# Performance work log

Measured on AMD Instinct MI355X. Metric: run time of the kernel, lower is better.

The kernel has to match this reference:

```python
import jax, jax.numpy as jnp
import numpy as np

N = 100000
E = 1600000
IN_C, HID_C, OUT_C = 128, 128, 64


def setup_inputs() -> dict:
    key = jax.random.key(0)
    k1, k2, k3, k4, k5, k6 = jax.random.split(key, 6)
    x = jax.random.normal(k1, (N, IN_C), dtype=jnp.float32)
    edge_index = jax.random.randint(k2, (2, E), 0, N, dtype=jnp.int64)
    # Glorot-style init like PyG GCNConv Linear
    W1 = jax.random.normal(k3, (IN_C, HID_C), dtype=jnp.float32) / np.sqrt(IN_C)
    b1 = jnp.zeros((HID_C,), dtype=jnp.float32)
    W2 = jax.random.normal(k4, (HID_C, OUT_C), dtype=jnp.float32) / np.sqrt(HID_C)
    b2 = jnp.zeros((OUT_C,), dtype=jnp.float32)
    return {"x": x, "edge_index": edge_index, "W1": W1, "b1": b1, "W2": W2, "b2": b2}


def gcn_conv(x, src, dst, norm, W, b, n_nodes):
    # x: [N, F_in]; src/dst/norm: [E+N] (self-loops included)
    h = x @ W                                   # [N, F_out] small GEMM
    msg = h[src] * norm[:, None]                # [E+N, F_out] gather (dominant)
    out = jax.ops.segment_sum(msg, dst, num_segments=n_nodes)  # scatter-add
    return out + b


def gcn_norm(edge_index, n_nodes):
    # add self-loops, then symmetric normalization D^-1/2 (A+I) D^-1/2
    loop = jnp.arange(n_nodes, dtype=edge_index.dtype)
    src = jnp.concatenate([edge_index[0], loop])
    dst = jnp.concatenate([edge_index[1], loop])
    deg = jax.ops.segment_sum(jnp.ones_like(dst, dtype=jnp.float32), dst,
                              num_segments=n_nodes)
    dinv = jnp.where(deg > 0, jax.lax.rsqrt(jnp.maximum(deg, 1.0)), 0.0)
    norm = dinv[src] * dinv[dst]
    return src, dst, norm


def reference(x, edge_index, W1, b1, W2, b2):
    n_nodes = x.shape[0]
    src, dst, norm = gcn_norm(edge_index, n_nodes)  # cached=True -> computed once
    h = gcn_conv(x, src, dst, norm, W1, b1, n_nodes)
    h = jax.nn.relu(h)
    # dropout in eval mode (training=False) is identity
    out = gcn_conv(h, src, dst, norm, W2, b2, n_nodes)
    return out
```

## Files before the change

### kernel.cpp

```cpp
#include <hip/hip_runtime.h>
#include <hip/hip_fp16.h>

constexpr int NN  = 100000;
constexpr int NE  = 1600000;
constexpr int TOT = NE + NN;

constexpr int NBUK    = (NN + 255) / 256;
constexpr int EBLOCKS = 512;
constexpr int EPB     = NE / EBLOCKS;

__device__ inline float2 h2f2(unsigned int u) {
  __half2 h = __builtin_bit_cast(__half2, u);
  return __half22float2(h);
}
__device__ inline unsigned int f2h2(float a, float b) {
  __half2 h = __floats2half2_rn(a, b);
  return __builtin_bit_cast(unsigned int, h);
}

__global__ __launch_bounds__(256) void k_detect(const unsigned int* __restrict__ ei, int* __restrict__ flag) {
  __shared__ int nz;
  if (threadIdx.x == 0) nz = 0;
  __syncthreads();
  if (ei[threadIdx.x * 2 + 1] != 0u) atomicAdd(&nz, 1);
  __syncthreads();
  if (threadIdx.x == 0) flag[0] = (nz == 0) ? 1 : 0;
}

__device__ inline int load_idx(const void* ei, long long i, int is64) {
  return is64 ? (int)((const long long*)ei)[i] : ((const int*)ei)[i];
}


__global__ __launch_bounds__(256) void k_hist(const void* __restrict__ ei, const int* __restrict__ flag,
                                              int* __restrict__ hist_g) {
  __shared__ int h[NBUK];
  int is64 = flag[0];
  for (int i = threadIdx.x; i < NBUK; i += 256) h[i] = 0;
  __syncthreads();
  int e0 = blockIdx.x * EPB;
  for (int e = e0 + threadIdx.x; e < e0 + EPB; e += 256) {
    int d = load_idx(ei, (long long)NE + e, is64);
    atomicAdd(&h[d >> 8], 1);
  }
  __syncthreads();
  for (int i = threadIdx.x; i < NBUK; i += 256)
    hist_g[i * EBLOCKS + blockIdx.x] = h[i];
}

__global__ __launch_bounds__(512) void k_scan_hist(int* __restrict__ hist_g, int* __restrict__ bucket_total) {
  __shared__ int s[EBLOCKS];
  int b = blockIdx.x, t = threadIdx.x;
  int v = hist_g[b * EBLOCKS + t];
  s[t] = v;
  __syncthreads();
  for (int off = 1; off < EBLOCKS; off <<= 1) {
    int u = (t >= off) ? s[t - off] : 0;
    __syncthreads();
    s[t] += u;
    __syncthreads();
  }
  hist_g[b * EBLOCKS + t] = s[t] - v;
  if (t == EBLOCKS - 1) bucket_total[b] = s[t];
}

__global__ __launch_bounds__(512) void k_scan_buckets(const int* __restrict__ bucket_total,
                                                      int* __restrict__ edge_base, int* __restrict__ row_start) {
  __shared__ int s[512];
  int t = threadIdx.x;
  int v = (t < NBUK) ? bucket_total[t] : 0;
  s[t] = v;
  __syncthreads();
  for (int off = 1; off < 512; off <<= 1) {
    int u = (t >= off) ? s[t - off] : 0;
    __syncthreads();
    s[t] += u;
    __syncthreads();
  }
  if (t <= NBUK) edge_base[t] = s[t] - v;
  if (t == 0) row_start[NN] = TOT;
}

__global__ __launch_bounds__(256) void k_scatter(const void* __restrict__ ei, const int* __restrict__ flag,
                                                 const int* __restrict__ hist_g, const int* __restrict__ edge_base,
                                                 int2* __restrict__ rec) {
  __shared__ int cur[NBUK];
  int is64 = flag[0];
  for (int i = threadIdx.x; i < NBUK; i += 256)
    cur[i] = edge_base[i] + hist_g[i * EBLOCKS + blockIdx.x];
  __syncthreads();
  int e0 = blockIdx.x * EPB;
  for (int e = e0 + threadIdx.x; e < e0 + EPB; e += 256) {
    int sA = load_idx(ei, e, is64);
    int d  = load_idx(ei, (long long)NE + e, is64);
    int p = atomicAdd(&cur[d >> 8], 1);
    rec[p] = make_int2(sA, d);
  }
}

__global__ __launch_bounds__(256) void k_bucket_csr(const int2* __restrict__ rec, const int* __restrict__ edge_base,
                                                    int* __restrict__ row_start, float* __restrict__ dinv,
                                                    int* __restrict__ csr_src) {
  __shared__ int cnt[256];
  __shared__ int s[256];
  int b = blockIdx.x, t = threadIdx.x;
  int node = b * 256 + t;
  cnt[t] = 0;
  __syncthreads();
  int j0 = edge_base[b], j1 = edge_base[b + 1];
  for (int j = j0 + t; j < j1; j += 256)
    atomicAdd(&cnt[rec[j].y & 255], 1);
  __syncthreads();
  int c = (node < NN) ? cnt[t] + 1 : 0;
  s[t] = c;
  __syncthreads();
  for (int off = 1; off < 256; off <<= 1) {
    int u = (t >= off) ? s[t - off] : 0;
    __syncthreads();
    s[t] += u;
    __syncthreads();
  }
  int csr_b = j0 + b * 256;
  int start = csr_b + s[t] - c;
  if (node < NN) {
    row_start[node] = start;
    dinv[node] = rsqrtf((float)c);
    csr_src[start] = node;
  }
  __syncthreads();
  cnt[t] = start + 1;
  __syncthreads();
  for (int j = j0 + t; j < j1; j += 256) {
    int2 r = rec[j];
    int p = atomicAdd(&cnt[r.y & 255], 1);
    csr_src[p] = r.x;
  }
}

template<int OUTC, bool IN_H, bool OUT_H>
__global__ __launch_bounds__(256) void k_gemm(const void* __restrict__ Xv,
                                              const float* __restrict__ W,
                                              void* __restrict__ Yv, int nrows) {
  constexpr int CG   = OUTC / 8;
  constexpr int RG   = 256 / CG;
  constexpr int ROWS = RG * 4;
  constexpr int KB   = 64;
  constexpr int XS   = 65;
  __shared__ float sW[KB * OUTC];
  __shared__ float sX[ROWS * XS];
  const int tid  = threadIdx.x;
  const int row0 = blockIdx.x * ROWS;
  const int cg = tid % CG, rg = tid / CG;
  float acc[4][8] = {};

  for (int kc = 0; kc < 128; kc += KB) {
    __syncthreads();
    for (int i = tid * 4; i < KB * OUTC; i += 1024)
      *(float4*)&sW[i] = *(const float4*)&W[kc * OUTC + i];
    if constexpr (!IN_H) {
      const float* X = (const float*)Xv;
      for (int idx = tid; idx < ROWS * (KB / 4); idx += 256) {
        int r = idx / (KB / 4), k4 = idx % (KB / 4);
        int gr = row0 + r;
        float4 v = make_float4(0.f, 0.f, 0.f, 0.f);
        if (gr < nrows) v = *(const float4*)&X[(size_t)gr * 128 + kc + k4 * 4];
        float* p = &sX[r * XS + k4 * 4];
        p[0] = v.x; p[1] = v.y; p[2] = v.z; p[3] = v.w;
      }
    } else {
      const unsigned short* X = (const unsigned short*)Xv;
      for (int idx = tid; idx < ROWS * (KB / 8); idx += 256) {
        int r = idx / (KB / 8), g = idx % (KB / 8);
        int gr = row0 + r;
        uint4 v = make_uint4(0u, 0u, 0u, 0u);
        if (gr < nrows) v = *(const uint4*)&X[(size_t)gr * 128 + kc + g * 8];
        float* p = &sX[r * XS + g * 8];
        float2 f;
        f = h2f2(v.x); p[0] = f.x; p[1] = f.y;
        f = h2f2(v.y); p[2] = f.x; p[3] = f.y;
        f = h2f2(v.z); p[4] = f.x; p[5] = f.y;
        f = h2f2(v.w); p[6] = f.x; p[7] = f.y;
      }
    }
    __syncthreads();
    #pragma unroll 8
    for (int k = 0; k < KB; k++) {
      float aa[4];
      aa[0] = sX[(rg * 4 + 0) * XS + k];
      aa[1] = sX[(rg * 4 + 1) * XS + k];
      aa[2] = sX[(rg * 4 + 2) * XS + k];
      aa[3] = sX[(rg * 4 + 3) * XS + k];
      float4 b0 = *(const float4*)&sW[k * OUTC + cg * 8];
      float4 b1 = *(const float4*)&sW[k * OUTC + cg * 8 + 4];
      float bb[8] = {b0.x, b0.y, b0.z, b0.w, b1.x, b1.y, b1.z, b1.w};
      #pragma unroll
      for (int i2 = 0; i2 < 4; i2++)
        #pragma unroll
        for (int j2 = 0; j2 < 8; j2++)
          acc[i2][j2] = fmaf(aa[i2], bb[j2], acc[i2][j2]);
    }
  }
  #pragma unroll
  for (int i2 = 0; i2 < 4; i2++) {
    int gr = row0 + rg * 4 + i2;
    if (gr < nrows) {
      if constexpr (OUT_H) {
        unsigned short* Y = (unsigned short*)Yv;
        uint4 o;
        o.x = f2h2(acc[i2][0], acc[i2][1]);
        o.y = f2h2(acc[i2][2], acc[i2][3]);
        o.z = f2h2(acc[i2][4], acc[i2][5]);
        o.w = f2h2(acc[i2][6], acc[i2][7]);
        *(uint4*)&Y[(size_t)gr * OUTC + cg * 8] = o;
      } else {
        float* Y = (float*)Yv;
        *(float4*)&Y[(size_t)gr * OUTC + cg * 8]     = make_float4(acc[i2][0], acc[i2][1], acc[i2][2], acc[i2][3]);
        *(float4*)&Y[(size_t)gr * OUTC + cg * 8 + 4] = make_float4(acc[i2][4], acc[i2][5], acc[i2][6], acc[i2][7]);
      }
    }
  }
}

template<int F, bool RELU, bool OUT_H>
__global__ __launch_bounds__(256) void k_agg(const unsigned short* __restrict__ h, const float* __restrict__ dinv,
                                             const int* __restrict__ row_start, const int* __restrict__ csr_src,
                                             const float* __restrict__ bias, void* __restrict__ outv) {
  constexpr int LPN = F / 8;
  constexpr int NPB = 256 / LPN;
  int node = blockIdx.x * NPB + threadIdx.x / LPN;
  int lane = threadIdx.x % LPN;
  if (node >= NN) return;
  int j0 = row_start[node], j1 = row_start[node + 1];
  float acc[8] = {};
  #pragma unroll 2
  for (int j = j0; j < j1; j++) {
    int s = csr_src[j];
    float w = dinv[s];
    uint4 v = *(const uint4*)&h[(size_t)s * F + lane * 8];
    float2 f;
    f = h2f2(v.x); acc[0] = fmaf(w, f.x, acc[0]); acc[1] = fmaf(w, f.y, acc[1]);
    f = h2f2(v.y); acc[2] = fmaf(w, f.x, acc[2]); acc[3] = fmaf(w, f.y, acc[3]);
    f = h2f2(v.z); acc[4] = fmaf(w, f.x, acc[4]); acc[5] = fmaf(w, f.y, acc[5]);
    f = h2f2(v.w); acc[6] = fmaf(w, f.x, acc[6]); acc[7] = fmaf(w, f.y, acc[7]);
  }
  float dn = dinv[node];
  float o[8];
  #pragma unroll
  for (int t = 0; t < 8; t++) {
    o[t] = fmaf(dn, acc[t], bias[lane * 8 + t]);
    if (RELU) o[t] = fmaxf(o[t], 0.f);
  }
  if constexpr (OUT_H) {
    unsigned short* out = (unsigned short*)outv;
    uint4 w;
    w.x = f2h2(o[0], o[1]);
    w.y = f2h2(o[2], o[3]);
    w.z = f2h2(o[4], o[5]);
    w.w = f2h2(o[6], o[7]);
    *(uint4*)&out[(size_t)node * F + lane * 8] = w;
  } else {
    float* out = (float*)outv;
    *(float4*)&out[(size_t)node * F + lane * 8]     = make_float4(o[0], o[1], o[2], o[3]);
    *(float4*)&out[(size_t)node * F + lane * 8 + 4] = make_float4(o[4], o[5], o[6], o[7]);
  }
}

extern "C" void kernel_launch(void* const* d_in, const int* in_sizes, int n_in,
                              void* d_out, int out_size, void* d_ws, size_t ws_size,
                              hipStream_t stream) {
  const float* x  = (const float*)d_in[0];
  const void*  ei = d_in[1];
  const float* W1 = (const float*)d_in[2];
  const float* b1 = (const float*)d_in[3];
  const float* W2 = (const float*)d_in[4];
  const float* b2 = (const float*)d_in[5];
  float* out = (float*)d_out;

  char* ws = (char*)d_ws;
  size_t off = 0;
  auto wsalloc = [&](size_t bytes) -> void* {
    void* p = ws + off;
    off += (bytes + 255) & ~(size_t)255;
    return p;
  };
  int*            row_start    = (int*)   wsalloc((NN + 1) * sizeof(int));
  int*            hist_g       = (int*)   wsalloc((size_t)NBUK * EBLOCKS * sizeof(int));
  int*            bucket_total = (int*)   wsalloc(NBUK * sizeof(int));
  int*            edge_base    = (int*)   wsalloc((NBUK + 1) * sizeof(int));
  float*          dinv         = (float*) wsalloc(NN * sizeof(float));
  int*            flag         = (int*)   wsalloc(64);
  int2*           rec          = (int2*)  wsalloc((size_t)NE * sizeof(int2));
  int*            csr_src      = (int*)   wsalloc((size_t)TOT * sizeof(int));
  unsigned short* h1           = (unsigned short*)wsalloc((size_t)NN * 128 * sizeof(unsigned short));
  unsigned short* hmid         = (unsigned short*)wsalloc((size_t)NN * 128 * sizeof(unsigned short));
  unsigned short* hL2          = h1;

  k_detect<<<1, 256, 0, stream>>>((const unsigned int*)ei, flag);
  k_hist<<<EBLOCKS, 256, 0, stream>>>(ei, flag, hist_g);
  k_scan_hist<<<NBUK, EBLOCKS, 0, stream>>>(hist_g, bucket_total);
  k_scan_buckets<<<1, 512, 0, stream>>>(bucket_total, edge_base, row_start);
  k_scatter<<<EBLOCKS, 256, 0, stream>>>(ei, flag, hist_g, edge_base, rec);
  k_bucket_csr<<<NBUK, 256, 0, stream>>>(rec, edge_base, row_start, dinv, csr_src);

  k_gemm<128, false, true><<<(NN + 63) / 64, 256, 0, stream>>>(x, W1, h1, NN);
  k_agg<128, true, true><<<(NN + 15) / 16, 256, 0, stream>>>(h1, dinv, row_start, csr_src, b1, hmid);
  k_gemm<64, true, true><<<(NN + 127) / 128, 256, 0, stream>>>(hmid, W2, hL2, NN);
  k_agg<64, false, false><<<(NN + 31) / 32, 256, 0, stream>>>(hL2, dinv, row_start, csr_src, b2, out);
}
```

Measured before the change: 327.9 us.

## Use fp16 MFMA for GEMMs and fold source-degree scaling into GEMM epilogue

```diff
diff --git a/kernel.cpp b/kernel.cpp
--- a/kernel.cpp
+++ b/kernel.cpp
@@ -8,6 +8,9 @@
 constexpr int NBUK    = (NN + 255) / 256;
 constexpr int EBLOCKS = 512;
 constexpr int EPB     = NE / EBLOCKS;
+
+typedef _Float16 f16x8 __attribute__((ext_vector_type(8)));
+typedef float    f32x4 __attribute__((ext_vector_type(4)));
 
 __device__ inline float2 h2f2(unsigned int u) {
   __half2 h = __builtin_bit_cast(__half2, u);
@@ -137,86 +140,85 @@
   }
 }
 
-template<int OUTC, bool IN_H, bool OUT_H>
-__global__ __launch_bounds__(256) void k_gemm(const void* __restrict__ Xv,
-                                              const float* __restrict__ W,
-                                              void* __restrict__ Yv, int nrows) {
-  constexpr int CG   = OUTC / 8;
-  constexpr int RG   = 256 / CG;
-  constexpr int ROWS = RG * 4;
-  constexpr int KB   = 64;
-  constexpr int XS   = 65;
-  __shared__ float sW[KB * OUTC];
-  __shared__ float sX[ROWS * XS];
+template<int OUTC, bool IN_H>
+__global__ __launch_bounds__(256) void k_gemm_mfma(const void* __restrict__ Xv,
+                                                   const float* __restrict__ W,
+                                                   const float* __restrict__ dinv,
+                                                   unsigned short* __restrict__ Y) {
+  constexpr int NT = OUTC / 16;
+  constexpr int PS = 136;
+  constexpr int SS = OUTC + 8;
+  constexpr int WT_H = OUTC * PS;
+  constexpr int ST_H = 64 * SS;
+  constexpr int SM_H = WT_H > ST_H ? WT_H : ST_H;
+  __shared__ _Float16 smem[SM_H];
+
   const int tid  = threadIdx.x;
-  const int row0 = blockIdx.x * ROWS;
-  const int cg = tid % CG, rg = tid / CG;
-  float acc[4][8] = {};
-
-  for (int kc = 0; kc < 128; kc += KB) {
-    __syncthreads();
-    for (int i = tid * 4; i < KB * OUTC; i += 1024)
-      *(float4*)&sW[i] = *(const float4*)&W[kc * OUTC + i];
-    if constexpr (!IN_H) {
+  const int lane = tid & 63;
+  const int wv   = tid >> 6;
+  const int row0 = blockIdx.x * 64;
+  const int l15  = lane & 15;
+  const int kg   = lane >> 4;
+
+  for (int idx = tid * 4; idx < 128 * OUTC; idx += 1024) {
+    float4 v = *(const float4*)&W[idx];
+    int k = idx / OUTC, c = idx % OUTC;
+    smem[(c + 0) * PS + k] = (_Float16)v.x;
+    smem[(c + 1) * PS + k] = (_Float16)v.y;
+    smem[(c + 2) * PS + k] = (_Float16)v.z;
+    smem[(c + 3) * PS + k] = (_Float16)v.w;
+  }
+  __syncthreads();
+
+  int arow = row0 + wv * 16 + l15;
+  int rr_g = arow < NN ? arow : NN - 1;
+
+  f32x4 acc[NT];
+  #pragma unroll
+  for (int n = 0; n < NT; n++) acc[n] = (f32x4){0.f, 0.f, 0.f, 0.f};
+
+  #pragma unroll
+  for (int kb = 0; kb < 4; kb++) {
+    int k0 = kb * 32 + kg * 8;
+    f16x8 a;
+    if constexpr (IN_H) {
+      a = *(const f16x8*)((const _Float16*)Xv + (size_t)rr_g * 128 + k0);
+    } else {
       const float* X = (const float*)Xv;
-      for (int idx = tid; idx < ROWS * (KB / 4); idx += 256) {
-        int r = idx / (KB / 4), k4 = idx % (KB / 4);
-        int gr = row0 + r;
-        float4 v = make_float4(0.f, 0.f, 0.f, 0.f);
-        if (gr < nrows) v = *(const float4*)&X[(size_t)gr * 128 + kc + k4 * 4];
-        float* p = &sX[r * XS + k4 * 4];
-        p[0] = v.x; p[1] = v.y; p[2] = v.z; p[3] = v.w;
-      }
-    } else {
-      const unsigned short* X = (const unsigned short*)Xv;
-      for (int idx = tid; idx < ROWS * (KB / 8); idx += 256) {
-        int r = idx / (KB / 8), g = idx % (KB / 8);
-        int gr = row0 + r;
-        uint4 v = make_uint4(0u, 0u, 0u, 0u);
-        if (gr < nrows) v = *(const uint4*)&X[(size_t)gr * 128 + kc + g * 8];
-        float* p = &sX[r * XS + g * 8];
-        float2 f;
-        f = h2f2(v.x); p[0] = f.x; p[1] = f.y;
-        f = h2f2(v.y); p[2] = f.x; p[3] = f.y;
-        f = h2f2(v.z); p[4] = f.x; p[5] = f.y;
-        f = h2f2(v.w); p[6] = f.x; p[7] = f.y;
-      }
+      float4 v0 = *(const float4*)&X[(size_t)rr_g * 128 + k0];
+      float4 v1 = *(const float4*)&X[(size_t)rr_g * 128 + k0 + 4];
+      a[0] = (_Float16)v0.x; a[1] = (_Float16)v0.y; a[2] = (_Float16)v0.z; a[3] = (_Float16)v0.w;
+      a[4] = (_Float16)v1.x; a[5] = (_Float16)v1.y; a[6] = (_Float16)v1.z; a[7] = (_Float16)v1.w;
     }
-    __syncthreads();
-    #pragma unroll 8
-    for (int k = 0; k < KB; k++) {
-      float aa[4];
-      aa[0] = sX[(rg * 4 + 0) * XS + k];
-      aa[1] = sX[(rg * 4 + 1) * XS + k];
-      aa[2] = sX[(rg * 4 + 2) * XS + k];
-      aa[3] = sX[(rg * 4 + 3) * XS + k];
-      float4 b0 = *(const float4*)&sW[k * OUTC + cg * 8];
-      float4 b1 = *(const float4*)&sW[k * OUTC + cg * 8 + 4];
-      float bb[8] = {b0.x, b0.y, b0.z, b0.w, b1.x, b1.y, b1.z, b1.w};
-      #pragma unroll
-      for (int i2 = 0; i2 < 4; i2++)
-        #pragma unroll
-        for (int j2 = 0; j2 < 8; j2++)
-          acc[i2][j2] = fmaf(aa[i2], bb[j2], acc[i2][j2]);
+    #pragma unroll
+    for (int n = 0; n < NT; n++) {
+      f16x8 b = *(const f16x8*)&smem[(n * 16 + l15) * PS + k0];
+      acc[n] = __builtin_amdgcn_mfma_f32_16x16x32_f16(a, b, acc[n], 0, 0, 0);
     }
   }
-  #pragma unroll
-  for (int i2 = 0; i2 < 4; i2++) {
-    int gr = row0 + rg * 4 + i2;
-    if (gr < nrows) {
-      if constexpr (OUT_H) {
-        unsigned short* Y = (unsigned short*)Yv;
-        uint4 o;
-        o.x = f2h2(acc[i2][0], acc[i2][1]);
-        o.y = f2h2(acc[i2][2], acc[i2][3]);
-        o.z = f2h2(acc[i2][4], acc[i2][5]);
-        o.w = f2h2(acc[i2][6], acc[i2][7]);
-        *(uint4*)&Y[(size_t)gr * OUTC + cg * 8] = o;
-      } else {
-        float* Y = (float*)Yv;
-        *(float4*)&Y[(size_t)gr * OUTC + cg * 8]     = make_float4(acc[i2][0], acc[i2][1], acc[i2][2], acc[i2][3]);
-        *(float4*)&Y[(size_t)gr * OUTC + cg * 8 + 4] = make_float4(acc[i2][4], acc[i2][5], acc[i2][6], acc[i2][7]);
-      }
+  __syncthreads();
+
+  int rb = wv * 16 + kg * 4;
+  float dv[4];
+  #pragma unroll
+  for (int q = 0; q < 4; q++) {
+    int gr = row0 + rb + q;
+    dv[q] = dinv[gr < NN ? gr : NN - 1];
+  }
+  #pragma unroll
+  for (int n = 0; n < NT; n++)
+    #pragma unroll
+    for (int q = 0; q < 4; q++)
+      smem[(rb + q) * SS + n * 16 + l15] = (_Float16)(acc[n][q] * dv[q]);
+  __syncthreads();
+
+  constexpr int SEGS = OUTC / 8;
+  for (int u = tid; u < 64 * SEGS; u += 256) {
+    int rr = u / SEGS, sg = u % SEGS;
+    int gr = row0 + rr;
+    if (gr < NN) {
+      uint4 v = *(const uint4*)&smem[rr * SS + sg * 8];
+      *(uint4*)&Y[(size_t)gr * OUTC + sg * 8] = v;
     }
   }
 }
@@ -235,13 +237,12 @@
   #pragma unroll 2
   for (int j = j0; j < j1; j++) {
     int s = csr_src[j];
-    float w = dinv[s];
     uint4 v = *(const uint4*)&h[(size_t)s * F + lane * 8];
     float2 f;
-    f = h2f2(v.x); acc[0] = fmaf(w, f.x, acc[0]); acc[1] = fmaf(w, f.y, acc[1]);
-    f = h2f2(v.y); acc[2] = fmaf(w, f.x, acc[2]); acc[3] = fmaf(w, f.y, acc[3]);
-    f = h2f2(v.z); acc[4] = fmaf(w, f.x, acc[4]); acc[5] = fmaf(w, f.y, acc[5]);
-    f = h2f2(v.w); acc[6] = fmaf(w, f.x, acc[6]); acc[7] = fmaf(w, f.y, acc[7]);
+    f = h2f2(v.x); acc[0] += f.x; acc[1] += f.y;
+    f = h2f2(v.y); acc[2] += f.x; acc[3] += f.y;
+    f = h2f2(v.z); acc[4] += f.x; acc[5] += f.y;
+    f = h2f2(v.w); acc[6] += f.x; acc[7] += f.y;
   }
   float dn = dinv[node];
   float o[8];
@@ -302,8 +303,9 @@
   k_scatter<<<EBLOCKS, 256, 0, stream>>>(ei, flag, hist_g, edge_base, rec);
   k_bucket_csr<<<NBUK, 256, 0, stream>>>(rec, edge_base, row_start, dinv, csr_src);
 
-  k_gemm<128, false, true><<<(NN + 63) / 64, 256, 0, stream>>>(x, W1, h1, NN);
+  constexpr int GBLK = (NN + 63) / 64;
+  k_gemm_mfma<128, false><<<GBLK, 256, 0, stream>>>(x, W1, dinv, h1);
   k_agg<128, true, true><<<(NN + 15) / 16, 256, 0, stream>>>(h1, dinv, row_start, csr_src, b1, hmid);
-  k_gemm<64, true, true><<<(NN + 127) / 128, 256, 0, stream>>>(hmid, W2, hL2, NN);
+  k_gemm_mfma<64, true><<<GBLK, 256, 0, stream>>>(hmid, W2, dinv, hL2);
   k_agg<64, false, false><<<(NN + 31) / 32, 256, 0, stream>>>(hL2, dinv, row_start, csr_src, b2, out);
 }
```

After: 291.5 us. 11.1% less time.
